# Kernel optimization log

Measured on AMD Instinct MI355X. Metric: run time of the kernel, lower is better.

The kernel has to match this reference:

```python
import jax, jax.numpy as jnp
import numpy as np

B, L, H, D = 2, 2048, 16, 64
HID = H * D
EPS = 1e-6


def setup_inputs() -> dict:
    key = jax.random.key(0)
    k1, k2, k3 = jax.random.split(key, 3)
    x = jax.random.normal(k1, (B, L, HID), dtype=jnp.float32)
    Wqkv = jax.random.normal(k2, (HID, 3 * HID), dtype=jnp.float32) * 0.02
    Wo = jax.random.normal(k3, (HID, HID), dtype=jnp.float32) * 0.02
    q_norm_w = jnp.ones((D,), dtype=jnp.float32)
    k_norm_w = jnp.ones((D,), dtype=jnp.float32)
    # real RoPE tables: (L, D/2)
    d2 = D // 2
    inv_freq = 1.0 / (10000.0 ** (np.arange(d2, dtype=np.float32) / d2))
    ang = np.arange(L, dtype=np.float32)[:, None] * inv_freq[None, :]
    cos = jnp.asarray(np.cos(ang), dtype=jnp.float32)
    sin = jnp.asarray(np.sin(ang), dtype=jnp.float32)
    return {"x": x, "Wqkv": Wqkv, "Wo": Wo, "q_norm_w": q_norm_w,
            "k_norm_w": k_norm_w, "cos": cos, "sin": sin}


def _rmsnorm(t, w, eps=EPS):
    # normalize over last (head_dim) axis
    var = jnp.mean(t * t, axis=-1, keepdims=True)
    return t * jax.lax.rsqrt(var + eps) * w


def _rope(t, cos, sin):
    # t: (B,H,L,D); cos,sin: (1,1,L,D/2)
    d2 = t.shape[-1] // 2
    t1, t2 = t[..., :d2], t[..., d2:]
    return jnp.concatenate([t1 * cos - t2 * sin, t1 * sin + t2 * cos], axis=-1)


def reference(x, Wqkv, Wo, q_norm_w, k_norm_w, cos, sin):
    Bx, Lx, _ = x.shape
    qkv = x @ Wqkv                                   # (B,L,3*HID)
    qkv = qkv.reshape(Bx, Lx, 3, H, D)
    q = jnp.transpose(qkv[:, :, 0], (0, 2, 1, 3))    # (B,H,L,D)
    k = jnp.transpose(qkv[:, :, 1], (0, 2, 1, 3))
    v = jnp.transpose(qkv[:, :, 2], (0, 2, 1, 3))
    q = _rmsnorm(q, q_norm_w)
    k = _rmsnorm(k, k_norm_w)
    c = cos[:Lx][None, None]                         # (1,1,L,D/2)
    s = sin[:Lx][None, None]
    q = _rope(q, c, s)
    k = _rope(k, c, s)
    scale = 1.0 / jnp.sqrt(jnp.float32(D))
    scores = jnp.einsum("bhqd,bhkd->bhqk", q, k) * scale
    causal = jnp.tril(jnp.ones((Lx, Lx), dtype=bool))
    scores = jnp.where(causal, scores, jnp.finfo(scores.dtype).min)
    attn = jax.nn.softmax(scores, axis=-1)
    out = jnp.einsum("bhqk,bhkd->bhqd", attn, v)     # (B,H,L,D)
    out = jnp.transpose(out, (0, 2, 1, 3)).reshape(Bx, Lx, HID)
    return out @ Wo
```

## Files before the change

### kernel.cpp

```cpp
#include <hip/hip_runtime.h>
#include <hip/hip_bf16.h>

typedef __attribute__((ext_vector_type(8))) short bh8;
typedef __attribute__((ext_vector_type(4))) float f4;

typedef unsigned short u16;
typedef unsigned int u32;

__device__ inline u16 f2b(float f) {
  __hip_bfloat16 h = __float2bfloat16(f);
  union { __hip_bfloat16 h; u16 u; } v; v.h = h; return v.u;
}
__device__ inline float b2f(u16 b) {
  union { u32 u; float f; } v; v.u = ((u32)b) << 16;
  return v.f;
}

__device__ __forceinline__ void gload16(const u16* g, u16* l) {
  __builtin_amdgcn_global_load_lds(
      (__attribute__((address_space(1))) void*)(g),
      (__attribute__((address_space(3))) void*)(l),
      16, 0, 0);
}

__global__ __launch_bounds__(256) void k_prep1(const float* __restrict__ x,
                                               const float* __restrict__ Wqkv,
                                               const float* __restrict__ Wo,
                                               u16* __restrict__ xb,
                                               u16* __restrict__ wqkvT,
                                               u16* __restrict__ woT) {
  int idx = blockIdx.x;
  if (idx < 4096) {
    int i = (idx * 256 + threadIdx.x) * 4;
    float4 v = *(const float4*)&x[i];
    ushort4 o;
    o.x = f2b(v.x); o.y = f2b(v.y); o.z = f2b(v.z); o.w = f2b(v.w);
    *(ushort4*)&xb[i] = o;
    return;
  }
  __shared__ u16 t[32][33];
  const float* W; u16* WT; int K, N, bxi, byi;
  if (idx < 7168) {
    int id2 = idx - 4096;
    W = Wqkv; WT = wqkvT; K = 1024; N = 3072;
    bxi = id2 % 96; byi = id2 / 96;
  } else {
    int id2 = idx - 7168;
    W = Wo; WT = woT; K = 1024; N = 1024;
    bxi = id2 & 31; byi = id2 >> 5;
  }
  int bx = bxi * 32, by = byi * 32;
  int xx = threadIdx.x & 31, yy = threadIdx.x >> 5;
  for (int j = 0; j < 4; ++j) {
    int r = yy + j * 8;
    t[r][xx] = f2b(W[(size_t)(by + r) * N + bx + xx]);
  }
  __syncthreads();
  for (int j = 0; j < 4; ++j) {
    int r = yy + j * 8;
    WT[(size_t)(bx + r) * K + by + xx] = t[xx][r];
  }
}

template <bool F32OUT>
__global__ __launch_bounds__(512, 2) void k_gemm256(const u16* __restrict__ A,
                                                    const u16* __restrict__ Bt,
                                                    void* __restrict__ Cout,
                                                    int M, int N, int K) {
  __shared__ u16 As[2][2][128 * 64];
  __shared__ u16 Bs[2][2][128 * 64];
  const int tid = threadIdx.x;
  const int lane = tid & 63, wid = tid >> 6;
  const int l15 = lane & 15, lg = lane >> 4;
  const int wm = wid >> 2, wn = wid & 3;

  int nwg = gridDim.x * gridDim.y;
  int bid = blockIdx.y * gridDim.x + blockIdx.x;
  int cpx = nwg >> 3;
  int swz = (bid & 7) * cpx + (bid >> 3);
  int bx = swz % gridDim.x, by = swz / gridDim.x;
  const int bm = bx * 256, bn = by * 256;

  f4 acc[8][4] = {};

  const int srow = wid * 16 + (lane >> 3);
  const int key0 = (lane >> 3) & 7;
  const int scol = ((lane & 7) ^ key0) * 8;

  const int nk = K >> 6;

#define STAGE256(T)                                                                   \
  {                                                                                   \
    int kb_ = (T) << 6; int bf_ = (T) & 1;                                            \
    _Pragma("unroll")                                                                 \
    for (int h = 0; h < 2; ++h) {                                                     \
      const u16* ga = A + (size_t)(bm + h * 128 + srow) * K + kb_ + scol;             \
      u16* la = &As[bf_][h][(wid * 16) * 64];                                         \
      gload16(ga, la);                                                                \
      gload16(ga + (size_t)8 * K, la + 8 * 64);                                       \
      const u16* gb = Bt + (size_t)(bn + h * 128 + srow) * K + kb_ + scol;            \
      u16* lb = &Bs[bf_][h][(wid * 16) * 64];                                         \
      gload16(gb, lb);                                                                \
      gload16(gb + (size_t)8 * K, lb + 8 * 64);                                       \
    }                                                                                 \
  }

#define QUAD256(T, MH, NH)                                                            \
  {                                                                                   \
    const u16* as_ = &As[(T) & 1][wm][0];                                             \
    const u16* bs_ = &Bs[(T) & 1][wn >> 1][0];                                        \
    bh8 a_[4][2], b_[2][2];                                                           \
    _Pragma("unroll")                                                                 \
    for (int i = 0; i < 4; ++i) {                                                     \
      int ar = ((MH) * 4 + i) * 16 + l15;                                             \
      _Pragma("unroll")                                                               \
      for (int kk = 0; kk < 2; ++kk)                                                  \
        a_[i][kk] = *(const bh8*)&as_[ar * 64 + (((kk * 4 + lg) ^ (ar & 7)) * 8)];    \
    }                                                                                 \
    _Pragma("unroll")                                                                 \
    for (int j = 0; j < 2; ++j) {                                                     \
      int br = (wn & 1) * 64 + ((NH) * 2 + j) * 16 + l15;                             \
      _Pragma("unroll")                                                               \
      for (int kk = 0; kk < 2; ++kk)                                                  \
        b_[j][kk] = *(const bh8*)&bs_[br * 64 + (((kk * 4 + lg) ^ (br & 7)) * 8)];    \
    }                                                                                 \
    asm volatile("s_waitcnt lgkmcnt(0)" ::: "memory");                                \
    __builtin_amdgcn_sched_barrier(0);                                                \
    __builtin_amdgcn_s_setprio(1);                                                    \
    _Pragma("unroll")                                                                 \
    for (int kk = 0; kk < 2; ++kk)                                                    \
      _Pragma("unroll")                                                               \
      for (int i = 0; i < 4; ++i)                                                     \
        _Pragma("unroll")                                                             \
        for (int j = 0; j < 2; ++j)                                                   \
          acc[(MH) * 4 + i][(NH) * 2 + j] = __builtin_amdgcn_mfma_f32_16x16x32_bf16(  \
              a_[i][kk], b_[j][kk], acc[(MH) * 4 + i][(NH) * 2 + j], 0, 0, 0);        \
    __builtin_amdgcn_s_setprio(0);                                                    \
  }

  STAGE256(0);
  __syncthreads();

  for (int t = 0; t < nk; ++t) {
    if (t + 1 < nk) STAGE256(t + 1);
    QUAD256(t, 0, 0);
    QUAD256(t, 0, 1);
    QUAD256(t, 1, 0);
    QUAD256(t, 1, 1);
    __syncthreads();
  }
#undef STAGE256
#undef QUAD256

  for (int mf = 0; mf < 8; ++mf)
    for (int nf = 0; nf < 4; ++nf)
      for (int r = 0; r < 4; ++r) {
        int row = bm + wm * 128 + mf * 16 + lg * 4 + r;
        int col = bn + wn * 64 + nf * 16 + l15;
        float v = acc[mf][nf][r];
        if constexpr (F32OUT) ((float*)Cout)[(size_t)row * N + col] = v;
        else                  ((u16*)Cout)[(size_t)row * N + col]  = f2b(v);
      }
}

template <bool F32OUT>
__global__ __launch_bounds__(256) void k_gemm(const u16* __restrict__ A,
                                              const u16* __restrict__ Bt,
                                              void* __restrict__ Cout,
                                              int M, int N, int K) {
  __shared__ u16 As[2][128 * 64];
  __shared__ u16 Bs[2][128 * 64];
  const int tid = threadIdx.x;
  const int lane = tid & 63, wid = tid >> 6;
  const int l15 = lane & 15, lg = lane >> 4;
  const int bm = blockIdx.x * 128, bn = blockIdx.y * 128;
  const int wr = (wid >> 1) * 64, wc = (wid & 1) * 64;

  f4 acc[4][4] = {};

  const int srow = wid * 32 + (lane >> 3);
  const int scol = ((lane & 7) ^ ((lane >> 3) & 7)) * 8;
  const u16* gA = A  + (size_t)(bm + srow) * K + scol;
  const u16* gB = Bt + (size_t)(bn + srow) * K + scol;

  const int nk = K >> 6;

  {
    const u16* ga = gA; const u16* gb = gB;
    u16* la = &As[0][(wid * 32) * 64];
    u16* lb = &Bs[0][(wid * 32) * 64];
    #pragma unroll
    for (int c = 0; c < 4; ++c) {
      gload16(ga, la);
      gload16(gb, lb);
      ga += (size_t)8 * K; gb += (size_t)8 * K;
      la += 8 * 64;        lb += 8 * 64;
    }
  }
  __syncthreads();

  for (int t = 0; t < nk; ++t) {
    if (t + 1 < nk) {
      int kb = (t + 1) << 6;
      const u16* ga = gA + kb; const u16* gb = gB + kb;
      u16* la = &As[(t + 1) & 1][(wid * 32) * 64];
      u16* lb = &Bs[(t + 1) & 1][(wid * 32) * 64];
      #pragma unroll
      for (int c = 0; c < 4; ++c) {
        gload16(ga, la);
        gload16(gb, lb);
        ga += (size_t)8 * K; gb += (size_t)8 * K;
        la += 8 * 64;        lb += 8 * 64;
      }
    }
    const u16* as = &As[t & 1][0];
    const u16* bs = &Bs[t & 1][0];
    #pragma unroll
    for (int kk = 0; kk < 2; ++kk) {
      bh8 a[4], b[4];
      #pragma unroll
      for (int m = 0; m < 4; ++m)
        a[m] = *(const bh8*)&as[(wr + m * 16 + l15) * 64 + (((kk * 4 + lg) ^ (l15 & 7)) * 8)];
      #pragma unroll
      for (int n = 0; n < 4; ++n)
        b[n] = *(const bh8*)&bs[(wc + n * 16 + l15) * 64 + (((kk * 4 + lg) ^ (l15 & 7)) * 8)];
      #pragma unroll
      for (int m = 0; m < 4; ++m)
        #pragma unroll
        for (int n = 0; n < 4; ++n)
          acc[m][n] = __builtin_amdgcn_mfma_f32_16x16x32_bf16(a[m], b[n], acc[m][n], 0, 0, 0);
    }
    __syncthreads();
  }

  for (int m = 0; m < 4; ++m)
    for (int n = 0; n < 4; ++n)
      for (int r = 0; r < 4; ++r) {
        int row = bm + wr + m * 16 + lg * 4 + r;
        int col = bn + wc + n * 16 + l15;
        float v = acc[m][n][r];
        if constexpr (F32OUT) ((float*)Cout)[(size_t)row * N + col] = v;
        else                  ((u16*)Cout)[(size_t)row * N + col]  = f2b(v);
      }
}

__global__ __launch_bounds__(256) void k_prep2(const u16* __restrict__ qkv,
                                               const float* __restrict__ qw,
                                               const float* __restrict__ kw,
                                               const float* __restrict__ cosp,
                                               const float* __restrict__ sinp,
                                               u16* __restrict__ Q,
                                               u16* __restrict__ K,
                                               u16* __restrict__ Vt) {
  const float CSC = 0.125f * 1.44269504088896f;
  int idx = blockIdx.x;
  if (idx < 2048) {
    int wid = threadIdx.x >> 6, lane = threadIdx.x & 63;
    int gw = idx * 4 + wid;
    int isK = gw & 1;
    int bl = gw >> 1;
    int l = bl & 2047, b = bl >> 11;
    int h = lane >> 2, qd = lane & 3;
    const u16* src = qkv + (size_t)bl * 3072 + isK * 1024 + h * 64 + qd * 8;
    bh8 t1 = *(const bh8*)src;
    bh8 t2 = *(const bh8*)(src + 32);
    float a1[8], a2[8];
    float ss = 0.0f;
    #pragma unroll
    for (int j = 0; j < 8; ++j) {
      a1[j] = b2f((u16)t1[j]); a2[j] = b2f((u16)t2[j]);
      ss += a1[j] * a1[j] + a2[j] * a2[j];
    }
    ss += __shfl_xor(ss, 1, 64);
    ss += __shfl_xor(ss, 2, 64);
    float rr = rsqrtf(ss * (1.0f / 64.0f) + 1e-6f);
    const float* wt = isK ? kw : qw;
    float w1[8], w2[8], cc[8], sn[8];
    *(float4*)&w1[0] = *(const float4*)&wt[qd * 8];
    *(float4*)&w1[4] = *(const float4*)&wt[qd * 8 + 4];
    *(float4*)&w2[0] = *(const float4*)&wt[32 + qd * 8];
    *(float4*)&w2[4] = *(const float4*)&wt[32 + qd * 8 + 4];
    *(float4*)&cc[0] = *(const float4*)&cosp[l * 32 + qd * 8];
    *(float4*)&cc[4] = *(const float4*)&cosp[l * 32 + qd * 8 + 4];
    *(float4*)&sn[0] = *(const float4*)&sinp[l * 32 + qd * 8];
    *(float4*)&sn[4] = *(const float4*)&sinp[l * 32 + qd * 8 + 4];
    float scl = isK ? 1.0f : CSC;
    bh8 o1, o2;
    #pragma unroll
    for (int j = 0; j < 8; ++j) {
      float x1 = a1[j] * rr * w1[j];
      float x2 = a2[j] * rr * w2[j];
      o1[j] = (short)f2b((x1 * cc[j] - x2 * sn[j]) * scl);
      o2[j] = (short)f2b((x1 * sn[j] + x2 * cc[j]) * scl);
    }
    u16* dst = (isK ? K : Q) + ((size_t)(b * 16 + h) * 2048 + l) * 64 + qd * 8;
    *(bh8*)dst = o1;
    *(bh8*)(dst + 32) = o2;
  } else {
    __shared__ u16 t[32][33];
    int v = idx - 2048;
    int bxi = v & 63, byi = (v >> 6) & 1, bh = v >> 7;
    int b = bh >> 4, h = bh & 15;
    int lb = bxi * 32, db = byi * 32;
    int xx = threadIdx.x & 31, yy = threadIdx.x >> 5;
    const u16* src = qkv + (size_t)b * 2048 * 3072 + 2048 + h * 64;
    for (int j = 0; j < 4; ++j) {
      int r = yy + j * 8;
      t[r][xx] = src[(size_t)(lb + r) * 3072 + db + xx];
    }
    __syncthreads();
    u16* dst = Vt + (size_t)bh * 64 * 2048;
    for (int j = 0; j < 4; ++j) {
      int r = yy + j * 8;
      dst[(size_t)(db + r) * 2048 + lb + xx] = t[xx][r];
    }
  }
}

__global__ __launch_bounds__(256, 3) void k_attn(const u16* __restrict__ Q,
                                                 const u16* __restrict__ K,
                                                 const u16* __restrict__ Vt,
                                                 u16* __restrict__ O,
                                                 u16* __restrict__ Opart,
                                                 float2* __restrict__ Ml) {
  __shared__ u16 Ks[2][64 * 64];
  __shared__ u16 Vs[2][64 * 64];
  __shared__ u16 Pl[4][32][64];

  const int bh = blockIdx.y;
  const int b = bh >> 4, h = bh & 15;
  const int wid = threadIdx.x >> 6, lane = threadIdx.x & 63;
  const int l15 = lane & 15, lg = lane >> 4;

  const int ctab[17] = {0,1,2,3,5,7,9,11,14,17,20,24,28,32,36,41,46};
  const int id = 45 - (int)blockIdx.x;
  int qt = 0;
  #pragma unroll
  for (int qq = 0; qq < 16; ++qq)
    if (id >= ctab[qq + 1]) qt = qq + 1;
  const int part = id - ctab[qt];
  const int ways = ctab[qt + 1] - ctab[qt];
  const int T = 2 * qt + 2;
  const int t0 = part * T / ways;
  const int t1 = (part + 1) * T / ways;
  const int slot = (ways == 1) ? -1 : bh * 43 + (id - 3);

  const int qb = qt * 128 + wid * 32;

  const u16* Qp = Q  + (size_t)bh * 2048 * 64;
  const u16* Kp = K  + (size_t)bh * 2048 * 64;
  const u16* Vp = Vt + (size_t)bh * 64 * 2048;

  const int sr0 = wid * 8 + (lane >> 3);
  const int sc  = lane & 7;

  bh8 aq[2][2];
  #pragma unroll
  for (int qi = 0; qi < 2; ++qi)
    #pragma unroll
    for (int hh = 0; hh < 2; ++hh)
      aq[qi][hh] = *(const bh8*)&Qp[(size_t)(qb + qi * 16 + l15) * 64 + hh * 32 + lg * 8];

  bh8 ones;
  #pragma unroll
  for (int j = 0; j < 8; ++j) ones[j] = (short)0x3F80;

  f4 acc[2][4] = {};
  float mrow[2] = {-1e30f, -1e30f};
  float lrow[2] = {0.0f, 0.0f};

  const int tmax = (qb + 31) >> 6;

  {
    int kb0 = t0 * 64;
    int r0 = sr0, r1 = 32 + sr0;
    gload16(Kp + (size_t)(kb0 + r0) * 64 + (size_t)((sc ^ (r0 & 7)) * 8), &Ks[t0 & 1][(wid * 8) * 64]);
    gload16(Kp + (size_t)(kb0 + r1) * 64 + (size_t)((sc ^ (r1 & 7)) * 8), &Ks[t0 & 1][(32 + wid * 8) * 64]);
    gload16(Vp + (size_t)r0 * 2048 + kb0 + (size_t)((sc ^ (r0 & 7)) * 8), &Vs[t0 & 1][(wid * 8) * 64]);
    gload16(Vp + (size_t)r1 * 2048 + kb0 + (size_t)((sc ^ (r1 & 7)) * 8), &Vs[t0 & 1][(32 + wid * 8) * 64]);
  }
  __syncthreads();

  for (int t = t0; t < t1; ++t) {
    if (t + 1 < t1) {
      int kb = (t + 1) * 64;
      int nb = (t + 1) & 1;
      int r0 = sr0, r1 = 32 + sr0;
      gload16(Kp + (size_t)(kb + r0) * 64 + (size_t)((sc ^ (r0 & 7)) * 8), &Ks[nb][(wid * 8) * 64]);
      gload16(Kp + (size_t)(kb + r1) * 64 + (size_t)((sc ^ (r1 & 7)) * 8), &Ks[nb][(32 + wid * 8) * 64]);
      gload16(Vp + (size_t)r0 * 2048 + kb + (size_t)((sc ^ (r0 & 7)) * 8), &Vs[nb][(wid * 8) * 64]);
      gload16(Vp + (size_t)r1 * 2048 + kb + (size_t)((sc ^ (r1 & 7)) * 8), &Vs[nb][(32 + wid * 8) * 64]);
    }
    if (t <= tmax) {
      const int kb = t * 64;
      const bool masked = (t == tmax);
      const u16* ks = &Ks[t & 1][0];
      const u16* vs = &Vs[t & 1][0];

      f4 sc4[4][2] = {};
      __builtin_amdgcn_s_setprio(1);
      #pragma unroll
      for (int kq = 0; kq < 4; ++kq) {
        int row = kq * 16 + l15;
        int cs = row & 7;
        bh8 ka0 = *(const bh8*)&ks[row * 64 + ((0 + lg) ^ cs) * 8];
        bh8 ka1 = *(const bh8*)&ks[row * 64 + ((4 + lg) ^ cs) * 8];
        #pragma unroll
        for (int qi = 0; qi < 2; ++qi) {
          sc4[kq][qi] = __builtin_amdgcn_mfma_f32_16x16x32_bf16(ka0, aq[qi][0], sc4[kq][qi], 0, 0, 0);
          sc4[kq][qi] = __builtin_amdgcn_mfma_f32_16x16x32_bf16(ka1, aq[qi][1], sc4[kq][qi], 0, 0, 0);
        }
      }
      __builtin_amdgcn_s_setprio(0);

      #pragma unroll
      for (int qi = 0; qi < 2; ++qi) {
        if (masked) {
          int q = qb + qi * 16 + l15;
          #pragma unroll
          for (int kq = 0; kq < 4; ++kq)
            #pragma unroll
            for (int r = 0; r < 4; ++r)
              if (kb + kq * 16 + lg * 4 + r > q) sc4[kq][qi][r] = -1e30f;
        }
        float mx = -1e30f;
        #pragma unroll
        for (int kq = 0; kq < 4; ++kq)
          #pragma unroll
          for (int r = 0; r < 4; ++r)
            mx = fmaxf(mx, sc4[kq][qi][r]);
        mx = fmaxf(mx, __shfl_xor(mx, 16, 64));
        mx = fmaxf(mx, __shfl_xor(mx, 32, 64));
        if (__any(mx > mrow[qi] + 8.0f)) {
          float mnew = fmaxf(mrow[qi], mx);
          float fac = exp2f(mrow[qi] - mnew);
          mrow[qi] = mnew;
          lrow[qi] *= fac;
          #pragma unroll
          for (int n = 0; n < 4; ++n)
            #pragma unroll
            for (int r = 0; r < 4; ++r) acc[qi][n][r] *= fac;
        }
        #pragma unroll
        for (int kq = 0; kq < 4; ++kq)
          #pragma unroll
          for (int r = 0; r < 4; ++r)
            sc4[kq][qi][r] = exp2f(sc4[kq][qi][r] - mrow[qi]);
      }

      char* plb = (char*)&Pl[wid][0][0];
      #pragma unroll
      for (int qi = 0; qi < 2; ++qi) {
        int row = qi * 16 + l15;
        #pragma unroll
        for (int kq = 0; kq < 4; ++kq) {
          ushort4 w4;
          w4.x = f2b(sc4[kq][qi][0]); w4.y = f2b(sc4[kq][qi][1]);
          w4.z = f2b(sc4[kq][qi][2]); w4.w = f2b(sc4[kq][qi][3]);
          int ch = (kq * 2 + (lg >> 1)) ^ (row & 7);
          *(ushort4*)(plb + row * 128 + ch * 16 + (lg & 1) * 8) = w4;
        }
      }
      asm volatile("s_waitcnt lgkmcnt(0)" ::: "memory");
      __builtin_amdgcn_sched_barrier(0);

      f4 sum0 = {}, sum1 = {};
      __builtin_amdgcn_s_setprio(1);
      #pragma unroll
      for (int g = 0; g < 2; ++g) {
        bh8 pb0 = *(const bh8*)(plb + l15 * 128 + (((g * 4 + lg) ^ (l15 & 7)) * 16));
        bh8 pb1 = *(const bh8*)(plb + (16 + l15) * 128 + (((g * 4 + lg) ^ (l15 & 7)) * 16));
        #pragma unroll
        for (int n = 0; n < 4; ++n) {
          int row = n * 16 + l15;
          bh8 va = *(const bh8*)&vs[row * 64 + (((g * 4 + lg) ^ (row & 7)) * 8)];
          acc[0][n] = __builtin_amdgcn_mfma_f32_16x16x32_bf16(va, pb0, acc[0][n], 0, 0, 0);
          acc[1][n] = __builtin_amdgcn_mfma_f32_16x16x32_bf16(va, pb1, acc[1][n], 0, 0, 0);
        }
        sum0 = __builtin_amdgcn_mfma_f32_16x16x32_bf16(ones, pb0, sum0, 0, 0, 0);
        sum1 = __builtin_amdgcn_mfma_f32_16x16x32_bf16(ones, pb1, sum1, 0, 0, 0);
      }
      __builtin_amdgcn_s_setprio(0);
      lrow[0] += sum0[0];
      lrow[1] += sum1[0];
    }
    __syncthreads();
  }

  if (slot < 0) {
    #pragma unroll
    for (int qi = 0; qi < 2; ++qi) {
      float inv = 1.0f / lrow[qi];
      int q = qb + qi * 16 + l15;
      #pragma unroll
      for (int n = 0; n < 4; ++n) {
        ushort4 w4;
        w4.x = f2b(acc[qi][n][0] * inv);
        w4.y = f2b(acc[qi][n][1] * inv);
        w4.z = f2b(acc[qi][n][2] * inv);
        w4.w = f2b(acc[qi][n][3] * inv);
        *(ushort4*)&O[((size_t)b * 2048 + q) * 1024 + h * 64 + n * 16 + lg * 4] = w4;
      }
    }
  } else {
    u16* op = Opart + (size_t)slot * 8192;
    #pragma unroll
    for (int qi = 0; qi < 2; ++qi) {
      int rloc = wid * 32 + qi * 16 + l15;
      #pragma unroll
      for (int n = 0; n < 4; ++n) {
        ushort4 w4;
        w4.x = f2b(acc[qi][n][0]); w4.y = f2b(acc[qi][n][1]);
        w4.z = f2b(acc[qi][n][2]); w4.w = f2b(acc[qi][n][3]);
        *(ushort4*)&op[(size_t)rloc * 64 + n * 16 + lg * 4] = w4;
      }
      if (lg == 0) Ml[slot * 128 + rloc] = make_float2(mrow[qi], lrow[qi]);
    }
  }
}

__global__ __launch_bounds__(256) void k_comb(const u16* __restrict__ Opart,
                                              const float2* __restrict__ Ml,
                                              u16* __restrict__ O) {
  const int ctab[17] = {0,1,2,3,5,7,9,11,14,17,20,24,28,32,36,41,46};
  int qt = 3 + (int)blockIdx.x;
  int bh = blockIdx.y;
  int b = bh >> 4, h = bh & 15;
  int ways = ctab[qt + 1] - ctab[qt];
  int base = bh * 43 + ctab[qt] - 3;
  int row = threadIdx.x >> 1;
  int db  = (threadIdx.x & 1) * 32;

  float2 ml[5]; float wgt[5];
  float M = -1e30f;
  #pragma unroll
  for (int w = 0; w < 5; ++w)
    if (w < ways) { ml[w] = Ml[(base + w) * 128 + row]; M = fmaxf(M, ml[w].x); }
  float l = 0.0f;
  #pragma unroll
  for (int w = 0; w < 5; ++w)
    if (w < ways) { wgt[w] = exp2f(ml[w].x - M); l += wgt[w] * ml[w].y; }
  float inv = 1.0f / l;

  u16* dst = O + ((size_t)b * 2048 + qt * 128 + row) * 1024 + h * 64 + db;
  #pragma unroll
  for (int j = 0; j < 32; j += 8) {
    float a[8] = {};
    #pragma unroll
    for (int w = 0; w < 5; ++w)
      if (w < ways) {
        bh8 v = *(const bh8*)&Opart[(size_t)(base + w) * 8192 + (size_t)row * 64 + db + j];
        #pragma unroll
        for (int e = 0; e < 8; ++e) a[e] += wgt[w] * b2f((u16)v[e]);
      }
    bh8 o;
    #pragma unroll
    for (int e = 0; e < 8; ++e) o[e] = (short)f2b(a[e] * inv);
    *(bh8*)&dst[j] = o;
  }
}

extern "C" void kernel_launch(void* const* d_in, const int* in_sizes, int n_in,
                              void* d_out, int out_size, void* d_ws, size_t ws_size,
                              hipStream_t stream) {
  (void)in_sizes; (void)n_in; (void)out_size; (void)ws_size;
  const float* x    = (const float*)d_in[0];
  const float* Wqkv = (const float*)d_in[1];
  const float* Wo   = (const float*)d_in[2];
  const float* qw   = (const float*)d_in[3];
  const float* kw   = (const float*)d_in[4];
  const float* cosp = (const float*)d_in[5];
  const float* sinp = (const float*)d_in[6];
  float* out = (float*)d_out;

  char* ws = (char*)d_ws;
  u16* xb    = (u16*)(ws);
  u16* wqkvT = (u16*)(ws + 8388608);
  u16* woT   = (u16*)(ws + 14680064);
  u16* qkv   = (u16*)(ws + 16777216);
  u16* Qb    = (u16*)(ws + 41943040);
  u16* Kb    = (u16*)(ws + 50331648);
  u16* Vtb   = (u16*)(ws + 58720256);
  u16* AO    = (u16*)(ws + 67108864);
  u16*    Opart = (u16*)(ws + 16777216);
  float2* Mlb   = (float2*)(ws + 16777216 + 22544384);

  k_prep1<<<8192, 256, 0, stream>>>(x, Wqkv, Wo, xb, wqkvT, woT);
  k_gemm256<false><<<dim3(16, 12), 512, 0, stream>>>(xb, wqkvT, qkv, 4096, 3072, 1024);
  k_prep2<<<6144, 256, 0, stream>>>(qkv, qw, kw, cosp, sinp, Qb, Kb, Vtb);
  k_attn<<<dim3(46, 32), 256, 0, stream>>>(Qb, Kb, Vtb, AO, Opart, Mlb);
  k_comb<<<dim3(13, 32), 256, 0, stream>>>(Opart, Mlb, AO);
  k_gemm<true><<<dim3(32, 8), 256, 0, stream>>>(AO, woT, out, 4096, 1024, 1024);
}
```

Measured before the change: 142.6 us.

## Halve attention P staging buffer, raise occupancy, vectorize V transpose

The attention kernel now stages the softmax probabilities through shared memory in two 32-key halves, which halves the per-wave P buffer. That saving allows launch bounds of 4 blocks per CU instead of 3, raising occupancy. It adds an extra wait and barrier between the halves. Separately, the V transpose in the prep kernel now handles 64x64 tiles with 16-byte vector loads and stores, so it launches half as many blocks. This trades some register budget per thread for the higher block count.

```diff
diff --git a/kernel.cpp b/kernel.cpp
--- a/kernel.cpp
+++ b/kernel.cpp
@@ -297,27 +297,30 @@
     *(bh8*)dst = o1;
     *(bh8*)(dst + 32) = o2;
   } else {
-    __shared__ u16 t[32][33];
+    __shared__ u16 tt[64][66];
     int v = idx - 2048;
-    int bxi = v & 63, byi = (v >> 6) & 1, bh = v >> 7;
+    int bh = v >> 5, lt = v & 31;
     int b = bh >> 4, h = bh & 15;
-    int lb = bxi * 32, db = byi * 32;
-    int xx = threadIdx.x & 31, yy = threadIdx.x >> 5;
+    int lb = lt * 64;
     const u16* src = qkv + (size_t)b * 2048 * 3072 + 2048 + h * 64;
-    for (int j = 0; j < 4; ++j) {
-      int r = yy + j * 8;
-      t[r][xx] = src[(size_t)(lb + r) * 3072 + db + xx];
-    }
+    int r0 = threadIdx.x >> 3, c0 = (threadIdx.x & 7) * 8;
+    *(bh8*)&tt[r0][c0]      = *(const bh8*)&src[(size_t)(lb + r0) * 3072 + c0];
+    *(bh8*)&tt[r0 + 32][c0] = *(const bh8*)&src[(size_t)(lb + r0 + 32) * 3072 + c0];
     __syncthreads();
     u16* dst = Vt + (size_t)bh * 64 * 2048;
-    for (int j = 0; j < 4; ++j) {
-      int r = yy + j * 8;
-      dst[(size_t)(db + r) * 2048 + lb + xx] = t[xx][r];
-    }
-  }
-}
-
-__global__ __launch_bounds__(256, 3) void k_attn(const u16* __restrict__ Q,
+    int d0 = threadIdx.x >> 3, l0 = (threadIdx.x & 7) * 8;
+    bh8 o0, o1;
+    #pragma unroll
+    for (int j = 0; j < 8; ++j) {
+      o0[j] = (short)tt[l0 + j][d0];
+      o1[j] = (short)tt[l0 + j][d0 + 32];
+    }
+    *(bh8*)&dst[(size_t)d0 * 2048 + lb + l0]        = o0;
+    *(bh8*)&dst[(size_t)(d0 + 32) * 2048 + lb + l0] = o1;
+  }
+}
+
+__global__ __launch_bounds__(256, 4) void k_attn(const u16* __restrict__ Q,
                                                  const u16* __restrict__ K,
                                                  const u16* __restrict__ Vt,
                                                  u16* __restrict__ O,
@@ -325,7 +328,7 @@
                                                  float2* __restrict__ Ml) {
   __shared__ u16 Ks[2][64 * 64];
   __shared__ u16 Vs[2][64 * 64];
-  __shared__ u16 Pl[4][32][64];
+  __shared__ u16 Pl[4][32][32];
 
   const int bh = blockIdx.y;
   const int b = bh >> 4, h = bh & 15;
@@ -449,27 +452,31 @@
       }
 
       char* plb = (char*)&Pl[wid][0][0];
-      #pragma unroll
-      for (int qi = 0; qi < 2; ++qi) {
-        int row = qi * 16 + l15;
+      f4 sum0 = {}, sum1 = {};
+      #pragma unroll
+      for (int g = 0; g < 2; ++g) {
+        if (g) {
+          asm volatile("s_waitcnt lgkmcnt(0)" ::: "memory");
+          __builtin_amdgcn_sched_barrier(0);
+        }
         #pragma unroll
-        for (int kq = 0; kq < 4; ++kq) {
-          ushort4 w4;
-          w4.x = f2b(sc4[kq][qi][0]); w4.y = f2b(sc4[kq][qi][1]);
-          w4.z = f2b(sc4[kq][qi][2]); w4.w = f2b(sc4[kq][qi][3]);
-          int ch = (kq * 2 + (lg >> 1)) ^ (row & 7);
-          *(ushort4*)(plb + row * 128 + ch * 16 + (lg & 1) * 8) = w4;
+        for (int qi = 0; qi < 2; ++qi) {
+          int row = qi * 16 + l15;
+          #pragma unroll
+          for (int kl = 0; kl < 2; ++kl) {
+            int kq = g * 2 + kl;
+            ushort4 w4;
+            w4.x = f2b(sc4[kq][qi][0]); w4.y = f2b(sc4[kq][qi][1]);
+            w4.z = f2b(sc4[kq][qi][2]); w4.w = f2b(sc4[kq][qi][3]);
+            int ch = (kl * 2 + (lg >> 1)) ^ (row & 3);
+            *(ushort4*)(plb + row * 64 + ch * 16 + (lg & 1) * 8) = w4;
+          }
         }
-      }
-      asm volatile("s_waitcnt lgkmcnt(0)" ::: "memory");
-      __builtin_amdgcn_sched_barrier(0);
-
-      f4 sum0 = {}, sum1 = {};
-      __builtin_amdgcn_s_setprio(1);
-      #pragma unroll
-      for (int g = 0; g < 2; ++g) {
-        bh8 pb0 = *(const bh8*)(plb + l15 * 128 + (((g * 4 + lg) ^ (l15 & 7)) * 16));
-        bh8 pb1 = *(const bh8*)(plb + (16 + l15) * 128 + (((g * 4 + lg) ^ (l15 & 7)) * 16));
+        asm volatile("s_waitcnt lgkmcnt(0)" ::: "memory");
+        __builtin_amdgcn_sched_barrier(0);
+        bh8 pb0 = *(const bh8*)(plb + l15 * 64 + ((lg ^ (l15 & 3)) * 16));
+        bh8 pb1 = *(const bh8*)(plb + (16 + l15) * 64 + ((lg ^ (l15 & 3)) * 16));
+        __builtin_amdgcn_s_setprio(1);
         #pragma unroll
         for (int n = 0; n < 4; ++n) {
           int row = n * 16 + l15;
@@ -479,8 +486,8 @@
         }
         sum0 = __builtin_amdgcn_mfma_f32_16x16x32_bf16(ones, pb0, sum0, 0, 0, 0);
         sum1 = __builtin_amdgcn_mfma_f32_16x16x32_bf16(ones, pb1, sum1, 0, 0, 0);
-      }
-      __builtin_amdgcn_s_setprio(0);
+        __builtin_amdgcn_s_setprio(0);
+      }
       lrow[0] += sum0[0];
       lrow[1] += sum1[0];
     }
@@ -587,7 +594,7 @@
 
   k_prep1<<<8192, 256, 0, stream>>>(x, Wqkv, Wo, xb, wqkvT, woT);
   k_gemm256<false><<<dim3(16, 12), 512, 0, stream>>>(xb, wqkvT, qkv, 4096, 3072, 1024);
-  k_prep2<<<6144, 256, 0, stream>>>(qkv, qw, kw, cosp, sinp, Qb, Kb, Vtb);
+  k_prep2<<<3072, 256, 0, stream>>>(qkv, qw, kw, cosp, sinp, Qb, Kb, Vtb);
   k_attn<<<dim3(46, 32), 256, 0, stream>>>(Qb, Kb, Vtb, AO, Opart, Mlb);
   k_comb<<<dim3(13, 32), 256, 0, stream>>>(Opart, Mlb, AO);
   k_gemm<true><<<dim3(32, 8), 256, 0, stream>>>(AO, woT, out, 4096, 1024, 1024);
```

Result: slower. 145.9 us (+2.3%).
